# Performance work log

Measured on AMD Instinct MI355X. Metric: run time of the kernel, lower is better.

## Reference

```python
import jax, jax.numpy as jnp
import numpy as np

B, S, E, H = 2, 2048, 1024, 16
D = E // H  # head_dim = 64


def setup_inputs() -> dict:
    key = jax.random.key(0)
    ks = jax.random.split(key, 6)
    scale = 1.0 / np.sqrt(E)
    x = jax.random.normal(ks[0], (B, S, E), dtype=jnp.float32)
    mask = jnp.ones((B, S), dtype=jnp.int32)
    Wqkv = jax.random.normal(ks[1], (E, 3 * E), dtype=jnp.float32) * scale
    bqkv = jax.random.normal(ks[2], (3 * E,), dtype=jnp.float32) * 0.01
    Wout = jax.random.normal(ks[3], (E, E), dtype=jnp.float32) * scale
    bout = jax.random.normal(ks[4], (E,), dtype=jnp.float32) * 0.01
    return {"x": x, "mask": mask, "Wqkv": Wqkv, "bqkv": bqkv, "Wout": Wout, "bout": bout}


def reference(x, mask, Wqkv, bqkv, Wout, bout):
    Bn, Sn, En = x.shape
    qkv = x @ Wqkv + bqkv                      # [B,S,3E]
    qkv = qkv.reshape(Bn, Sn, 3, H, D)
    qkv = jnp.transpose(qkv, (2, 0, 3, 1, 4))  # [3,B,H,S,D]
    q, k, v = qkv[0], qkv[1], qkv[2]
    scores = jnp.einsum('bhqd,bhkd->bhqk', q, k) / np.sqrt(D).astype(np.float32)
    m = mask[:, None, None, :]                 # [B,1,1,S]
    scores = jnp.where(m == 0, jnp.float32(-jnp.inf), scores)
    attn = jax.nn.softmax(scores, axis=-1)
    out = jnp.einsum('bhqk,bhkd->bhqd', attn, v)  # [B,H,S,D]
    out = jnp.transpose(out, (0, 2, 1, 3)).reshape(Bn, Sn, En)
    return out @ Wout + bout
```

## Files before the change

### kernel.cpp

```cpp
#include <hip/hip_runtime.h>


typedef __attribute__((ext_vector_type(8))) short short8;
typedef __attribute__((ext_vector_type(4))) float floatx4;
typedef unsigned short ushort_t;

static __device__ __forceinline__ ushort_t f2bf(float f) {
    unsigned u = __float_as_uint(f);
    u += 0x7fffu + ((u >> 16) & 1u);
    return (ushort_t)(u >> 16);
}
static __device__ __forceinline__ float bf2f(ushort_t h) {
    return __uint_as_float(((unsigned)h) << 16);
}
#if __has_builtin(__builtin_amdgcn_cvt_pk_bf16_f32)
typedef __attribute__((ext_vector_type(2))) __bf16 bf16x2_t;
static __device__ __forceinline__ unsigned pack2bf(float a, float b) {
    bf16x2_t r = __builtin_amdgcn_cvt_pk_bf16_f32(a, b);
    return __builtin_bit_cast(unsigned, r);
}
#else
static __device__ __forceinline__ unsigned pack2bf(float a, float b) {
    return (unsigned)f2bf(a) | ((unsigned)f2bf(b) << 16);
}
#endif
static __device__ __forceinline__ float hexp2(float x) {
    return __builtin_amdgcn_exp2f(x);
}
static __device__ __forceinline__ void gload16(const void* g, void* l) {
    __builtin_amdgcn_global_load_lds(
        (const __attribute__((address_space(1))) unsigned int*)g,
        (__attribute__((address_space(3))) unsigned int*)l, 16, 0, 0);
}

__global__ __launch_bounds__(256) void conv_hi(const float* __restrict__ in,
                                               ushort_t* __restrict__ out) {
    int i = blockIdx.x * 256 + threadIdx.x;
    float4 v = ((const float4*)in)[i];
    uint2 o;
    o.x = pack2bf(v.x, v.y);
    o.y = pack2bf(v.z, v.w);
    ((uint2*)out)[i] = o;
}

__global__ __launch_bounds__(256) void conv_T_hi(const float* __restrict__ W,
                                                 ushort_t* __restrict__ hiT,
                                                 int K, int N) {
    __shared__ float tile[32][33];
    const int nb = blockIdx.x * 32, kb = blockIdx.y * 32;
    const int t = threadIdx.x;
    const int r = t >> 3, c4 = (t & 7) * 4;
    float4 v = *(const float4*)&W[(size_t)(kb + r) * N + nb + c4];
    tile[r][c4 + 0] = v.x; tile[r][c4 + 1] = v.y;
    tile[r][c4 + 2] = v.z; tile[r][c4 + 3] = v.w;
    __syncthreads();
    uint2 o;
    o.x = pack2bf(tile[c4 + 0][r], tile[c4 + 1][r]);
    o.y = pack2bf(tile[c4 + 2][r], tile[c4 + 3][r]);
    size_t off = ((size_t)(nb + r) * K + kb + c4) >> 2;
    ((uint2*)hiT)[off] = o;
}

__global__ __launch_bounds__(256) void conv_madd(const int* __restrict__ mask,
                                                 float* __restrict__ maddg) {
    int i = blockIdx.x * 256 + threadIdx.x;
    maddg[i] = (mask[i] ? 0.f : -1e30f) - 24.0f;
}

__global__ __launch_bounds__(256, 3) void gemm_qkv(
    const ushort_t* __restrict__ A, const ushort_t* __restrict__ B,
    const float* __restrict__ bias, ushort_t* __restrict__ qkvb,
    ushort_t* __restrict__ vtg)
{
    const int K = 1024;
    __shared__ ushort_t Ah[128][32], Bh[128][32];
    const int bn = blockIdx.x * 128, bm = blockIdx.y * 128;
    const int t = threadIdx.x, w = t >> 6, lane = t & 63;
    const int l15 = lane & 15, quad = lane >> 4;
    const int wm = w >> 1, wn = w & 1;

    const int srow = w * 32 + (lane >> 2);
    const int skp  = (lane & 3) ^ ((lane >> 2) & 3);
    const int scol = skp * 8;
    const ushort_t* ga = A + (size_t)(bm + srow) * K + scol;
    const ushort_t* gb = B + (size_t)(bn + srow) * K + scol;
    const size_t rstep = (size_t)16 * K;
    const int fcol = ((quad ^ (l15 & 3)) * 8);

    floatx4 acc[4][4];
    #pragma unroll
    for (int mt = 0; mt < 4; ++mt)
        #pragma unroll
        for (int nt = 0; nt < 4; ++nt) acc[mt][nt] = (floatx4){0.f, 0.f, 0.f, 0.f};

    for (int k0 = 0; k0 < K; k0 += 32) {
        #pragma unroll
        for (int i = 0; i < 2; ++i) {
            gload16(ga + i * rstep + k0, &Ah[w * 32 + i * 16][0]);
            gload16(gb + i * rstep + k0, &Bh[w * 32 + i * 16][0]);
        }
        __syncthreads();
        short8 ah[4], bh[4];
        #pragma unroll
        for (int x = 0; x < 4; ++x) {
            ah[x] = *(const short8*)&Ah[wm * 64 + x * 16 + l15][fcol];
            bh[x] = *(const short8*)&Bh[wn * 64 + x * 16 + l15][fcol];
        }
        #pragma unroll
        for (int mt = 0; mt < 4; ++mt)
            #pragma unroll
            for (int nt = 0; nt < 4; ++nt)
                acc[mt][nt] = __builtin_amdgcn_mfma_f32_16x16x32_bf16(ah[mt], bh[nt], acc[mt][nt], 0, 0, 0);
        __syncthreads();
    }

    if (bn < 2048) {
        #pragma unroll
        for (int mt = 0; mt < 4; ++mt)
            #pragma unroll
            for (int r = 0; r < 4; ++r) {
                size_t row = (size_t)(bm + wm * 64 + mt * 16 + quad * 4 + r) * 2048;
                #pragma unroll
                for (int nt = 0; nt < 4; ++nt) {
                    int col = bn + wn * 64 + nt * 16 + l15;
                    qkvb[row + col] = f2bf(acc[mt][nt][r] + bias[col]);
                }
            }
    } else {
        const int h = (bn - 2048 + wn * 64) >> 6;
        #pragma unroll
        for (int mt = 0; mt < 4; ++mt) {
            int brow = bm + wm * 64 + mt * 16 + quad * 4;
            int b = brow >> 11, s = brow & 2047;
            #pragma unroll
            for (int nt = 0; nt < 4; ++nt) {
                int col = bn + wn * 64 + nt * 16 + l15;
                int d = nt * 16 + l15;
                float bv = bias[col];
                uint2 pk;
                pk.x = pack2bf(acc[mt][nt][0] + bv, acc[mt][nt][1] + bv);
                pk.y = pack2bf(acc[mt][nt][2] + bv, acc[mt][nt][3] + bv);
                *(uint2*)&vtg[((size_t)((b * 16 + h) * 64 + d)) * 2048 + s] = pk;
            }
        }
    }
}

__global__ __launch_bounds__(256, 3) void gemm_bf16_f32_64(
    const ushort_t* __restrict__ A, const ushort_t* __restrict__ B,
    const float* __restrict__ bias, float* __restrict__ C,
    int M, int N, int K)
{
    __shared__ ushort_t Ah[64][32], Bh[128][32];
    const int bn = blockIdx.x * 128, bm = blockIdx.y * 64;
    const int t = threadIdx.x, w = t >> 6, lane = t & 63;
    const int l15 = lane & 15, quad = lane >> 4;
    const int wm = w >> 1, wn = w & 1;

    const int srow = w * 16 + (lane >> 2);
    const int skp  = (lane & 3) ^ ((lane >> 2) & 3);
    const int scol = skp * 8;
    const ushort_t* ga  = A + (size_t)(bm + srow) * K + scol;
    const ushort_t* gb0 = B + (size_t)(bn + srow) * K + scol;
    const ushort_t* gb1 = B + (size_t)(bn + 64 + srow) * K + scol;
    const int fcol = ((quad ^ (l15 & 3)) * 8);

    floatx4 acc[2][4];
    #pragma unroll
    for (int mt = 0; mt < 2; ++mt)
        #pragma unroll
        for (int nt = 0; nt < 4; ++nt) acc[mt][nt] = (floatx4){0.f, 0.f, 0.f, 0.f};

    for (int k0 = 0; k0 < K; k0 += 32) {
        gload16(ga  + k0, &Ah[w * 16][0]);
        gload16(gb0 + k0, &Bh[w * 16][0]);
        gload16(gb1 + k0, &Bh[64 + w * 16][0]);
        __syncthreads();
        short8 ah[2], bh[4];
        #pragma unroll
        for (int x = 0; x < 2; ++x)
            ah[x] = *(const short8*)&Ah[wm * 32 + x * 16 + l15][fcol];
        #pragma unroll
        for (int x = 0; x < 4; ++x)
            bh[x] = *(const short8*)&Bh[wn * 64 + x * 16 + l15][fcol];
        #pragma unroll
        for (int mt = 0; mt < 2; ++mt)
            #pragma unroll
            for (int nt = 0; nt < 4; ++nt)
                acc[mt][nt] = __builtin_amdgcn_mfma_f32_16x16x32_bf16(ah[mt], bh[nt], acc[mt][nt], 0, 0, 0);
        __syncthreads();
    }
    #pragma unroll
    for (int mt = 0; mt < 2; ++mt)
        #pragma unroll
        for (int r = 0; r < 4; ++r) {
            size_t row = (size_t)(bm + wm * 32 + mt * 16 + quad * 4 + r) * N;
            #pragma unroll
            for (int nt = 0; nt < 4; ++nt) {
                int col = bn + wn * 64 + nt * 16 + l15;
                C[row + col] = acc[mt][nt][r] + bias[col];
            }
        }
}

__global__ __launch_bounds__(256, 2) void flash_v6(
    const ushort_t* __restrict__ qkv, const ushort_t* __restrict__ vtg,
    const float* __restrict__ maddg, ushort_t* __restrict__ attn)
{
    __shared__ ushort_t Ks[2][64][64];
    __shared__ ushort_t Vt[2][64][64];
    __shared__ ushort_t Ps[4][2][16][72];
    __shared__ float MaddL[2048];

    const int blk = blockIdx.x;
    const int xcd = blk & 7, rr = blk >> 3;
    const int qi = rr & 15, g = xcd + 8 * (rr >> 4);
    const int b = g >> 4, h = g & 15, q0 = qi * 128;

    const int t = threadIdx.x, wave = t >> 6, lane = t & 63;
    const int l15 = lane & 15, quad = lane >> 4;
    const size_t bS = (size_t)b * 2048;
    const float c1 = 0.125f * 1.44269504088896340736f;

    short8 qf[2][2];
    #pragma unroll
    for (int tt = 0; tt < 2; ++tt) {
        int q = q0 + wave * 32 + tt * 16 + l15;
        const ushort_t* qp = qkv + (bS + q) * 2048 + h * 64;
        qf[tt][0] = *(const short8*)(qp + quad * 8);
        qf[tt][1] = *(const short8*)(qp + 32 + quad * 8);
    }

    const int srow  = wave * 16 + (lane >> 3);
    const int schnk = ((lane & 7) ^ ((lane >> 3) & 7)) * 8;
    const ushort_t* gK = qkv + (bS + srow) * 2048 + 1024 + h * 64 + schnk;
    const ushort_t* gV = vtg + ((size_t)(b * 16 + h) * 64 + srow) * 2048 + schnk;

    gload16(gK,            &Ks[0][wave * 16][0]);
    gload16(gK + 8 * 2048, &Ks[0][wave * 16 + 8][0]);
    gload16(gV,            &Vt[0][wave * 16][0]);
    gload16(gV + 8 * 2048, &Vt[0][wave * 16 + 8][0]);
    {
        const float* gM = maddg + b * 2048 + wave * 512 + lane * 4;
        gload16(gM,       &MaddL[wave * 512]);
        gload16(gM + 256, &MaddL[wave * 512 + 256]);
    }
    __syncthreads();

    floatx4 outacc[2][4];
    float lsum[2] = {0.f, 0.f};
    #pragma unroll
    for (int tt = 0; tt < 2; ++tt)
        #pragma unroll
        for (int dt = 0; dt < 4; ++dt) outacc[tt][dt] = (floatx4){0.f, 0.f, 0.f, 0.f};

    int cur = 0;
    for (int kt = 0; kt < 32; ++kt) {
        const int k0 = kt * 64;
        {
            const int kn = (kt + 1 < 32) ? (kt + 1) * 64 : 0;
            const int nb = cur ^ 1;
            gload16(gK + (size_t)kn * 2048,            &Ks[nb][wave * 16][0]);
            gload16(gK + (size_t)(kn + 8) * 2048,      &Ks[nb][wave * 16 + 8][0]);
            gload16(gV + kn,                           &Vt[nb][wave * 16][0]);
            gload16(gV + kn + 8 * 2048,                &Vt[nb][wave * 16 + 8][0]);
        }

        short8 kf[2][4], vf[2][4];
        #pragma unroll
        for (int kc = 0; kc < 2; ++kc)
            #pragma unroll
            for (int c = 0; c < 4; ++c) {
                int ch = ((kc * 4 + quad) ^ (l15 & 7)) * 8;
                kf[kc][c] = *(const short8*)&Ks[cur][c * 16 + l15][ch];
                vf[kc][c] = *(const short8*)&Vt[cur][c * 16 + l15][ch];
            }
        float4 madd4[4];
        #pragma unroll
        for (int c = 0; c < 4; ++c)
            madd4[c] = *(const float4*)&MaddL[k0 + c * 16 + quad * 4];

        #pragma unroll
        for (int tt = 0; tt < 2; ++tt) {
            floatx4 sc[4];
            #pragma unroll
            for (int c = 0; c < 4; ++c) {
                sc[c] = (floatx4){0.f, 0.f, 0.f, 0.f};
                sc[c] = __builtin_amdgcn_mfma_f32_16x16x32_bf16(kf[0][c], qf[tt][0], sc[c], 0, 0, 0);
                sc[c] = __builtin_amdgcn_mfma_f32_16x16x32_bf16(kf[1][c], qf[tt][1], sc[c], 0, 0, 0);
            }
            #pragma unroll
            for (int c = 0; c < 4; ++c) {
                float p0 = hexp2(fmaf(sc[c][0], c1, madd4[c].x));
                float p1 = hexp2(fmaf(sc[c][1], c1, madd4[c].y));
                float p2 = hexp2(fmaf(sc[c][2], c1, madd4[c].z));
                float p3 = hexp2(fmaf(sc[c][3], c1, madd4[c].w));
                lsum[tt] += (p0 + p1) + (p2 + p3);
                uint2 pk;
                pk.x = pack2bf(p0, p1);
                pk.y = pack2bf(p2, p3);
                *(uint2*)&Ps[wave][tt][l15][c * 16 + quad * 4] = pk;
            }
            short8 pf0 = *(const short8*)&Ps[wave][tt][l15][quad * 8];
            short8 pf1 = *(const short8*)&Ps[wave][tt][l15][32 + quad * 8];
            #pragma unroll
            for (int dt = 0; dt < 4; ++dt) {
                outacc[tt][dt] = __builtin_amdgcn_mfma_f32_16x16x32_bf16(vf[0][dt], pf0, outacc[tt][dt], 0, 0, 0);
                outacc[tt][dt] = __builtin_amdgcn_mfma_f32_16x16x32_bf16(vf[1][dt], pf1, outacc[tt][dt], 0, 0, 0);
            }
        }
        __syncthreads();
        cur ^= 1;
    }

    #pragma unroll
    for (int tt = 0; tt < 2; ++tt) {
        lsum[tt] += __shfl_xor(lsum[tt], 16);
        lsum[tt] += __shfl_xor(lsum[tt], 32);
        float inv = 1.f / lsum[tt];
        int q = q0 + wave * 32 + tt * 16 + l15;
        ushort_t* orow = attn + (bS + q) * 1024 + h * 64;
        #pragma unroll
        for (int dt = 0; dt < 4; ++dt) {
            uint2 pk;
            pk.x = pack2bf(outacc[tt][dt][0] * inv, outacc[tt][dt][1] * inv);
            pk.y = pack2bf(outacc[tt][dt][2] * inv, outacc[tt][dt][3] * inv);
            *(uint2*)&orow[dt * 16 + quad * 4] = pk;
        }
    }
}

extern "C" void kernel_launch(void* const* d_in, const int* in_sizes, int n_in,
                              void* d_out, int out_size, void* d_ws, size_t ws_size,
                              hipStream_t stream) {
    const float* x    = (const float*)d_in[0];
    const int*   mask = (const int*)  d_in[1];
    const float* Wqkv = (const float*)d_in[2];
    const float* bqkv = (const float*)d_in[3];
    const float* Wout = (const float*)d_in[4];
    const float* bout = (const float*)d_in[5];
    float* out = (float*)d_out;

    char* ws = (char*)d_ws;
    ushort_t* xb    = (ushort_t*)(ws);
    ushort_t* wqT   = (ushort_t*)(ws + 8388608);
    ushort_t* qkvb  = (ushort_t*)(ws + 14680064);
    ushort_t* vtg   = (ushort_t*)(ws + 31457280);
    ushort_t* attnb = (ushort_t*)(ws + 39845888);
    ushort_t* woT   = (ushort_t*)(ws + 48234496);
    float*    maddg = (float*)   (ws + 50331648);

    const int M = 4096, E = 1024, N3 = 3072, S = 2048;

    conv_hi<<<dim3(M * E / 1024), dim3(256), 0, stream>>>(x, xb);
    conv_T_hi<<<dim3(N3 / 32, E / 32), dim3(256), 0, stream>>>(Wqkv, wqT, E, N3);
    conv_madd<<<dim3(M / 256), dim3(256), 0, stream>>>(mask, maddg);

    gemm_qkv<<<dim3(N3 / 128, M / 128), dim3(256), 0, stream>>>(
        xb, wqT, bqkv, qkvb, vtg);

    flash_v6<<<dim3(512), dim3(256), 0, stream>>>(qkvb, vtg, maddg, attnb);

    conv_T_hi<<<dim3(E / 32, E / 32), dim3(256), 0, stream>>>(Wout, woT, E, E);

    gemm_bf16_f32_64<<<dim3(E / 128, M / 64), dim3(256), 0, stream>>>(
        attnb, woT, bout, out, M, E, E);
}
```

Before: 208.2 us.

## Fuse prep conversions into one launch and stage V transpose through LDS

The four preprocessing kernels (x to bf16, the Wqkv and Wout transposes, and the mask additive bias) are merged into one kernel that picks its task from the block index. This cuts three kernel launches and moves the Wout conversion ahead of the attention kernel. Separately, the V-transpose epilogue of the QKV GEMM now writes tiles into a padded shared-memory buffer and then issues coalesced 16-byte row stores, replacing the strided 8-byte scattered stores. The cost is extra shared memory per block, which could reduce occupancy, plus additional barriers in the epilogue.

```diff
diff --git a/kernel.cpp b/kernel.cpp
--- a/kernel.cpp
+++ b/kernel.cpp
@@ -33,38 +33,53 @@
         (__attribute__((address_space(3))) unsigned int*)l, 16, 0, 0);
 }
 
-__global__ __launch_bounds__(256) void conv_hi(const float* __restrict__ in,
-                                               ushort_t* __restrict__ out) {
-    int i = blockIdx.x * 256 + threadIdx.x;
-    float4 v = ((const float4*)in)[i];
-    uint2 o;
-    o.x = pack2bf(v.x, v.y);
-    o.y = pack2bf(v.z, v.w);
-    ((uint2*)out)[i] = o;
-}
-
-__global__ __launch_bounds__(256) void conv_T_hi(const float* __restrict__ W,
-                                                 ushort_t* __restrict__ hiT,
-                                                 int K, int N) {
+__global__ __launch_bounds__(256) void prep(
+    const float* __restrict__ x, ushort_t* __restrict__ xb,
+    const float* __restrict__ Wqkv, ushort_t* __restrict__ wqT,
+    const float* __restrict__ Wout, ushort_t* __restrict__ woT,
+    const int* __restrict__ mask, float* __restrict__ maddg)
+{
     __shared__ float tile[32][33];
-    const int nb = blockIdx.x * 32, kb = blockIdx.y * 32;
+    const int bk = blockIdx.x;
     const int t = threadIdx.x;
-    const int r = t >> 3, c4 = (t & 7) * 4;
-    float4 v = *(const float4*)&W[(size_t)(kb + r) * N + nb + c4];
-    tile[r][c4 + 0] = v.x; tile[r][c4 + 1] = v.y;
-    tile[r][c4 + 2] = v.z; tile[r][c4 + 3] = v.w;
-    __syncthreads();
-    uint2 o;
-    o.x = pack2bf(tile[c4 + 0][r], tile[c4 + 1][r]);
-    o.y = pack2bf(tile[c4 + 2][r], tile[c4 + 3][r]);
-    size_t off = ((size_t)(nb + r) * K + kb + c4) >> 2;
-    ((uint2*)hiT)[off] = o;
-}
-
-__global__ __launch_bounds__(256) void conv_madd(const int* __restrict__ mask,
-                                                 float* __restrict__ maddg) {
-    int i = blockIdx.x * 256 + threadIdx.x;
-    maddg[i] = (mask[i] ? 0.f : -1e30f) - 24.0f;
+    if (bk < 4096) {
+        int i = bk * 256 + t;
+        float4 v = ((const float4*)x)[i];
+        uint2 o;
+        o.x = pack2bf(v.x, v.y);
+        o.y = pack2bf(v.z, v.w);
+        ((uint2*)xb)[i] = o;
+        return;
+    }
+    if (bk < 8192) {
+        const float* W; ushort_t* WT; int K, N, id;
+        if (bk < 7168) { W = Wqkv; WT = wqT; K = 1024; N = 3072; id = bk - 4096;
+                         int nb = (id % 96) * 32, kb = (id / 96) * 32;
+                         const int r = t >> 3, c4 = (t & 7) * 4;
+                         float4 v = *(const float4*)&W[(size_t)(kb + r) * N + nb + c4];
+                         tile[r][c4+0]=v.x; tile[r][c4+1]=v.y; tile[r][c4+2]=v.z; tile[r][c4+3]=v.w;
+                         __syncthreads();
+                         uint2 o;
+                         o.x = pack2bf(tile[c4+0][r], tile[c4+1][r]);
+                         o.y = pack2bf(tile[c4+2][r], tile[c4+3][r]);
+                         ((uint2*)WT)[((size_t)(nb + r) * K + kb + c4) >> 2] = o;
+        } else {         W = Wout; WT = woT; K = 1024; N = 1024; id = bk - 7168;
+                         int nb = (id % 32) * 32, kb = (id / 32) * 32;
+                         const int r = t >> 3, c4 = (t & 7) * 4;
+                         float4 v = *(const float4*)&W[(size_t)(kb + r) * N + nb + c4];
+                         tile[r][c4+0]=v.x; tile[r][c4+1]=v.y; tile[r][c4+2]=v.z; tile[r][c4+3]=v.w;
+                         __syncthreads();
+                         uint2 o;
+                         o.x = pack2bf(tile[c4+0][r], tile[c4+1][r]);
+                         o.y = pack2bf(tile[c4+2][r], tile[c4+3][r]);
+                         ((uint2*)WT)[((size_t)(nb + r) * K + kb + c4) >> 2] = o;
+        }
+        return;
+    }
+    {
+        int i = (bk - 8192) * 256 + t;
+        maddg[i] = (mask[i] ? 0.f : -1e30f) - 24.0f;
+    }
 }
 
 __global__ __launch_bounds__(256, 3) void gemm_qkv(
@@ -74,6 +89,7 @@
 {
     const int K = 1024;
     __shared__ ushort_t Ah[128][32], Bh[128][32];
+    __shared__ ushort_t Tb[64][136];
     const int bn = blockIdx.x * 128, bm = blockIdx.y * 128;
     const int t = threadIdx.x, w = t >> 6, lane = t & 63;
     const int l15 = lane & 15, quad = lane >> 4;
@@ -127,21 +143,34 @@
                 }
             }
     } else {
-        const int h = (bn - 2048 + wn * 64) >> 6;
-        #pragma unroll
-        for (int mt = 0; mt < 4; ++mt) {
-            int brow = bm + wm * 64 + mt * 16 + quad * 4;
-            int b = brow >> 11, s = brow & 2047;
-            #pragma unroll
-            for (int nt = 0; nt < 4; ++nt) {
-                int col = bn + wn * 64 + nt * 16 + l15;
-                int d = nt * 16 + l15;
-                float bv = bias[col];
-                uint2 pk;
-                pk.x = pack2bf(acc[mt][nt][0] + bv, acc[mt][nt][1] + bv);
-                pk.y = pack2bf(acc[mt][nt][2] + bv, acc[mt][nt][3] + bv);
-                *(uint2*)&vtg[((size_t)((b * 16 + h) * 64 + d)) * 2048 + s] = pk;
-            }
+        const int h0 = (bn - 2048) >> 6;
+        const int b  = bm >> 11, s0 = bm & 2047;
+        #pragma unroll
+        for (int hh = 0; hh < 2; ++hh) {
+            if (wn == hh) {
+                #pragma unroll
+                for (int mt = 0; mt < 4; ++mt)
+                    #pragma unroll
+                    for (int nt = 0; nt < 4; ++nt) {
+                        int d = nt * 16 + l15;
+                        int sb = wm * 64 + mt * 16 + quad * 4;
+                        float bv = bias[bn + hh * 64 + nt * 16 + l15];
+                        uint2 pk;
+                        pk.x = pack2bf(acc[mt][nt][0] + bv, acc[mt][nt][1] + bv);
+                        pk.y = pack2bf(acc[mt][nt][2] + bv, acc[mt][nt][3] + bv);
+                        *(uint2*)&Tb[d][sb] = pk;
+                    }
+            }
+            __syncthreads();
+            ushort_t* vbase = vtg + ((size_t)((b * 16 + h0 + hh) * 64)) * 2048 + s0;
+            #pragma unroll
+            for (int it = 0; it < 4; ++it) {
+                int idx = t + it * 256;
+                int d = idx >> 4, ch = idx & 15;
+                uint4 v = *(const uint4*)&Tb[d][ch * 8];
+                *(uint4*)&vbase[(size_t)d * 2048 + ch * 8] = v;
+            }
+            __syncthreads();
         }
     }
 }
@@ -350,19 +379,16 @@
     ushort_t* woT   = (ushort_t*)(ws + 48234496);
     float*    maddg = (float*)   (ws + 50331648);
 
-    const int M = 4096, E = 1024, N3 = 3072, S = 2048;
-
-    conv_hi<<<dim3(M * E / 1024), dim3(256), 0, stream>>>(x, xb);
-    conv_T_hi<<<dim3(N3 / 32, E / 32), dim3(256), 0, stream>>>(Wqkv, wqT, E, N3);
-    conv_madd<<<dim3(M / 256), dim3(256), 0, stream>>>(mask, maddg);
+    const int M = 4096, E = 1024, N3 = 3072;
+
+    prep<<<dim3(8208), dim3(256), 0, stream>>>(
+        x, xb, Wqkv, wqT, Wout, woT, mask, maddg);
 
     gemm_qkv<<<dim3(N3 / 128, M / 128), dim3(256), 0, stream>>>(
         xb, wqT, bqkv, qkvb, vtg);
 
     flash_v6<<<dim3(512), dim3(256), 0, stream>>>(qkvb, vtg, maddg, attnb);
 
-    conv_T_hi<<<dim3(E / 32, E / 32), dim3(256), 0, stream>>>(Wout, woT, E, E);
-
     gemm_bf16_f32_64<<<dim3(E / 128, M / 64), dim3(256), 0, stream>>>(
         attnb, woT, bout, out, M, E, E);
 }
```

Result: faster. 200.7 us (-3.6%).
